# Optimization experiments

Hardware: AMD Instinct MI355X
Metric: run time of the kernel (lower is better)

Reference implementation:

```python
import jax, jax.numpy as jnp
import numpy as np

MAX_ITER = 20
F_TOL = 1e-6
FREE_NUM = 64  # free_idx[1] + 1
TRUNC = (0, 512)  # truncate_idx


def setup_inputs() -> dict:
    key = jax.random.key(0)
    ks = jax.random.split(key, 8)
    bsz, in_dim, hid, out_dim, m = 1024, 512, 1024, 256, 128
    return {
        "b_primal": jax.random.normal(ks[0], (bsz, in_dim), jnp.float32),
        "W0": jax.random.normal(ks[1], (hid, in_dim), jnp.float32) / np.sqrt(in_dim).astype(np.float32),
        "b0": jnp.zeros((hid,), jnp.float32),
        "W1": jax.random.normal(ks[2], (hid, hid), jnp.float32) / np.sqrt(hid).astype(np.float32),
        "b1": jnp.zeros((hid,), jnp.float32),
        "W2": jax.random.normal(ks[3], (out_dim, hid), jnp.float32) / np.sqrt(hid).astype(np.float32),
        "b2": jnp.zeros((out_dim,), jnp.float32),
        "A": jax.random.normal(ks[4], (m, out_dim), jnp.float32) * 0.1,
        "b_vec": jax.random.normal(ks[5], (m,), jnp.float32),
        # scaled so spectral norm < 1 -> contracting fixed-point iteration
        "WzProj": jax.random.normal(ks[6], (out_dim, out_dim), jnp.float32) * 0.03,
        "WbProj": jax.random.normal(ks[7], (out_dim, m), jnp.float32) * 0.1,
    }


def reference(b_primal, W0, b0, W1, b1, W2, b2, A, b_vec, WzProj, WbProj):
    # eval-mode forward of DualNN (report_projection=True)
    x = b_primal[:, TRUNC[0]:TRUNC[1]]
    h = jax.nn.relu(x @ W0.T + b0)
    h = jax.nn.relu(h @ W1.T + b1)
    out = h @ W2.T + b2                      # [bsz, output_dim]

    bias_proj = b_vec @ WbProj.T             # [output_dim]

    def cond(state):
        _, it, res = state
        return (it <= MAX_ITER) & (res > F_TOL)

    def body(state):
        z, it, _ = state
        z = bias_proj + z @ WzProj.T         # affine projection step
        u = z[:, :FREE_NUM]
        v = jax.nn.relu(z[:, FREE_NUM:])     # clamp non-free coordinates
        z = jnp.concatenate([u, v], axis=-1)
        res = jnp.max(jnp.abs(z @ A.T - b_vec))  # inf-norm equality residual
        return z, it + 1, res

    z_star, curr_iter, _ = jax.lax.while_loop(
        cond, body, (out, jnp.int32(1), jnp.float32(jnp.inf)))
    return (z_star, out, curr_iter)
```

## Files before the change

### kernel.cpp

```cpp
#include <hip/hip_runtime.h>

typedef __attribute__((ext_vector_type(8))) __bf16 bf16x8;
typedef __attribute__((ext_vector_type(4))) float f32x4;

#define MAX_ITER_N 20
#define F_TOL_F 1e-6f
#define FREE_NUM_N 64

#define BSZ 1024
#define IN_DIM 512
#define HID 1024
#define OUT_DIM 256
#define M_CON 128

#define WS_BAR   0
#define WS_RES   8
#define WS_BP    48
#define WS_H1    304
#define WS_H2    (WS_H1 + 524288)
#define WS_APC   (WS_H2 + 524288)
#define WS_W0C   (WS_APC + 262144)
#define WS_W1C   (WS_W0C + 262144)
#define WS_W2C   (WS_W1C + 524288)
#define WS_WZG   (WS_W2C + 131072)
#define WS_AG    (WS_WZG + 32768)

__device__ __forceinline__ unsigned short f2bf(float f) {
    unsigned int u = __float_as_uint(f);
    u += 0x7fffu + ((u >> 16) & 1u);
    return (unsigned short)(u >> 16);
}

__device__ __forceinline__ void gload_lds16(const unsigned short* g, unsigned short* l) {
    __builtin_amdgcn_global_load_lds(
        (const __attribute__((address_space(1))) unsigned int*)(const void*)g,
        (__attribute__((address_space(3))) unsigned int*)(void*)l, 16, 0, 0);
}

__global__ __launch_bounds__(256) void prep_k(
    const float* __restrict__ b_primal, const float* __restrict__ W0,
    const float* __restrict__ W1, const float* __restrict__ W2,
    const float* __restrict__ Wz, const float* __restrict__ Am,
    const float* __restrict__ b_vec, const float* __restrict__ WbProj,
    float* __restrict__ ws)
{
    unsigned short* APc = (unsigned short*)(ws + WS_APC);
    unsigned short* W0c = (unsigned short*)(ws + WS_W0C);
    unsigned short* W1c = (unsigned short*)(ws + WS_W1C);
    unsigned short* W2c = (unsigned short*)(ws + WS_W2C);
    unsigned short* WzG = (unsigned short*)(ws + WS_WZG);
    unsigned short* AG  = (unsigned short*)(ws + WS_AG);
    float* bp = ws + WS_BP;

    int b = blockIdx.x;
    int tid = threadIdx.x;
    if (b >= 2400) {
        if (tid < 48) ((unsigned int*)ws)[tid] = 0u;
        float s = 0.0f;
        for (int k = 0; k < M_CON; ++k) s += b_vec[k] * WbProj[tid * M_CON + k];
        bp[tid] = s;
        return;
    }
    const float* src; unsigned short* dst; int off;
    if (b < 512)       { src = b_primal; dst = APc; off = b; }
    else if (b < 1024) { src = W0; dst = W0c; off = b - 512; }
    else if (b < 2048) { src = W1; dst = W1c; off = b - 1024; }
    else if (b < 2304) { src = W2; dst = W2c; off = b - 2048; }
    else if (b < 2368) { src = Wz; dst = WzG; off = b - 2304; }
    else               { src = Am; dst = AG;  off = b - 2368; }
    int idx = off * 1024 + tid * 4;
    float4 v = *(const float4*)(src + idx);
    ushort4 o;
    o.x = f2bf(v.x); o.y = f2bf(v.y); o.z = f2bf(v.z); o.w = f2bf(v.w);
    *(ushort4*)(dst + idx) = o;
}

__device__ __forceinline__ bf16x8 frag128(const unsigned short* lds, int row, int gc) {
    int phys = gc ^ (row & 15);
    return __builtin_bit_cast(bf16x8, *(const uint4*)(lds + row * 128 + phys * 8));
}

template<int K, int NTN, bool RELU, bool F32OUT>
__global__ __launch_bounds__(256, 2) void gemm64_k(
    const unsigned short* __restrict__ A,
    const unsigned short* __restrict__ B,
    const float* __restrict__ bias,
    void* __restrict__ Cv, int N_)
{
    constexpr int NCH = K / 128;
    __shared__ __align__(16) unsigned short As[2][64 * 128];
    __shared__ __align__(16) unsigned short Bs[2][64 * 128];

    const int tid = threadIdx.x;
    const int w = tid >> 6;
    const int lane = tid & 63;
    const int ln = lane & 15;
    const int q  = lane >> 4;
    const int wr = w >> 1;
    const int wc = w & 1;
    const int row0 = (blockIdx.x / NTN) * 64;
    const int col0 = (blockIdx.x % NTN) * 64;
    const unsigned short* Ab = A + row0 * K;
    const unsigned short* Bb = B + col0 * K;

    int soff[4], dbase[4];
#pragma unroll
    for (int i = 0; i < 4; ++i) {
        int P = w * 256 + i * 64 + lane;
        int row = P >> 4, pgc = P & 15;
        soff[i]  = row * K + (pgc ^ (row & 15)) * 8;
        dbase[i] = (w * 256 + i * 64) * 8;
    }

    f32x4 acc[2][2];
#pragma unroll
    for (int rm = 0; rm < 2; ++rm)
#pragma unroll
        for (int cn = 0; cn < 2; ++cn)
            acc[rm][cn] = (f32x4){0.f, 0.f, 0.f, 0.f};

#pragma unroll
    for (int i = 0; i < 4; ++i) {
        gload_lds16(Ab + soff[i], &As[0][dbase[i]]);
        gload_lds16(Bb + soff[i], &Bs[0][dbase[i]]);
    }

    for (int c = 0; c < NCH; ++c) {
        __syncthreads();
        if (c + 1 < NCH) {
            const unsigned short* Ak = Ab + (c + 1) * 128;
            const unsigned short* Bk = Bb + (c + 1) * 128;
            int nb = (c + 1) & 1;
#pragma unroll
            for (int i = 0; i < 4; ++i) {
                gload_lds16(Ak + soff[i], &As[nb][dbase[i]]);
                gload_lds16(Bk + soff[i], &Bs[nb][dbase[i]]);
            }
        }
        const unsigned short* Ac = As[c & 1];
        const unsigned short* Bc = Bs[c & 1];
#pragma unroll
        for (int ks = 0; ks < 4; ++ks) {
            bf16x8 af0 = frag128(Ac, wr * 32 + ln,      ks * 4 + q);
            bf16x8 af1 = frag128(Ac, wr * 32 + 16 + ln, ks * 4 + q);
            bf16x8 bf0 = frag128(Bc, wc * 32 + ln,      ks * 4 + q);
            bf16x8 bf1 = frag128(Bc, wc * 32 + 16 + ln, ks * 4 + q);
            acc[0][0] = __builtin_amdgcn_mfma_f32_16x16x32_bf16(af0, bf0, acc[0][0], 0, 0, 0);
            acc[0][1] = __builtin_amdgcn_mfma_f32_16x16x32_bf16(af0, bf1, acc[0][1], 0, 0, 0);
            acc[1][0] = __builtin_amdgcn_mfma_f32_16x16x32_bf16(af1, bf0, acc[1][0], 0, 0, 0);
            acc[1][1] = __builtin_amdgcn_mfma_f32_16x16x32_bf16(af1, bf1, acc[1][1], 0, 0, 0);
        }
    }

#pragma unroll
    for (int cn = 0; cn < 2; ++cn) {
        const int cc = col0 + wc * 32 + cn * 16 + ln;
        const float bv = bias[cc];
#pragma unroll
        for (int rm = 0; rm < 2; ++rm)
#pragma unroll
            for (int i = 0; i < 4; ++i) {
                int r = row0 + wr * 32 + rm * 16 + q * 4 + i;
                float v = acc[rm][cn][i] + bv;
                if (RELU) v = fmaxf(v, 0.0f);
                if (F32OUT) ((float*)Cv)[r * N_ + cc] = v;
                else ((unsigned short*)Cv)[r * N_ + cc] = f2bf(v);
            }
    }
}

template<int K, int NTN, bool RELU, bool F32OUT>
__global__ __launch_bounds__(256, 4) void gemm32_k(
    const unsigned short* __restrict__ A,
    const unsigned short* __restrict__ B,
    const float* __restrict__ bias,
    void* __restrict__ Cv, int N_)
{
    constexpr int NCH = K / 128;
    __shared__ __align__(16) unsigned short As[2][32 * 128];
    __shared__ __align__(16) unsigned short Bs[2][32 * 128];

    const int tid = threadIdx.x;
    const int w = tid >> 6;
    const int lane = tid & 63;
    const int ln = lane & 15;
    const int q  = lane >> 4;
    const int wr = w >> 1;
    const int wc = w & 1;
    const int row0 = (blockIdx.x / NTN) * 32;
    const int col0 = (blockIdx.x % NTN) * 32;
    const unsigned short* Ab = A + row0 * K;
    const unsigned short* Bb = B + col0 * K;

    int soff[2], dbase[2];
#pragma unroll
    for (int i = 0; i < 2; ++i) {
        int P = w * 128 + i * 64 + lane;
        int row = P >> 4, pgc = P & 15;
        soff[i]  = row * K + (pgc ^ (row & 15)) * 8;
        dbase[i] = (w * 128 + i * 64) * 8;
    }

    f32x4 acc = {0.f, 0.f, 0.f, 0.f};

#pragma unroll
    for (int i = 0; i < 2; ++i) {
        gload_lds16(Ab + soff[i], &As[0][dbase[i]]);
        gload_lds16(Bb + soff[i], &Bs[0][dbase[i]]);
    }

    for (int c = 0; c < NCH; ++c) {
        __syncthreads();
        if (c + 1 < NCH) {
            const unsigned short* Ak = Ab + (c + 1) * 128;
            const unsigned short* Bk = Bb + (c + 1) * 128;
            int nb = (c + 1) & 1;
#pragma unroll
            for (int i = 0; i < 2; ++i) {
                gload_lds16(Ak + soff[i], &As[nb][dbase[i]]);
                gload_lds16(Bk + soff[i], &Bs[nb][dbase[i]]);
            }
        }
        const unsigned short* Ac = As[c & 1];
        const unsigned short* Bc = Bs[c & 1];
#pragma unroll
        for (int ks = 0; ks < 4; ++ks) {
            bf16x8 af = frag128(Ac, wr * 16 + ln, ks * 4 + q);
            bf16x8 bf = frag128(Bc, wc * 16 + ln, ks * 4 + q);
            acc = __builtin_amdgcn_mfma_f32_16x16x32_bf16(af, bf, acc, 0, 0, 0);
        }
    }

    const int c = col0 + wc * 16 + ln;
    const float bv = bias[c];
#pragma unroll
    for (int i = 0; i < 4; ++i) {
        int r = row0 + wr * 16 + q * 4 + i;
        float v = acc[i] + bv;
        if (RELU) v = fmaxf(v, 0.0f);
        if (F32OUT) ((float*)Cv)[r * N_ + c] = v;
        else ((unsigned short*)Cv)[r * N_ + c] = f2bf(v);
    }
}

__global__ __launch_bounds__(256, 1) void loop_k(
    const float* __restrict__ b_vec, const float* __restrict__ WzProj,
    float* __restrict__ out, float* __restrict__ ws)
{
    __shared__ __align__(16) unsigned char smem[16 * 257 * 4 + 64];
    unsigned int* done = (unsigned int*)ws;
    unsigned int* res = (unsigned int*)(ws + WS_RES);
    float* bp = ws + WS_BP;
    const unsigned short* WzG = (const unsigned short*)(ws + WS_WZG);
    const unsigned short* AG  = (const unsigned short*)(ws + WS_AG);
    float* outz = out + BSZ * OUT_DIM;

    const int tid  = threadIdx.x;
    const int wave = tid >> 6;
    const int lane = tid & 63;
    const int ln   = lane & 15;
    const int q    = lane >> 4;
    const int r0   = blockIdx.x * 16;

    unsigned short (*zS)[264] = (unsigned short(*)[264])smem;
    float* red = (float*)(smem + 16 * 257 * 4);

    {
        int row = tid >> 4;
        int c0  = (tid & 15) * 16;
        const float* src = outz + (r0 + row) * OUT_DIM + c0;
#pragma unroll
        for (int i = 0; i < 4; ++i) {
            float4 v = *(const float4*)(src + i * 4);
            ushort4 o;
            o.x = f2bf(v.x); o.y = f2bf(v.y); o.z = f2bf(v.z); o.w = f2bf(v.w);
            *(ushort4*)&zS[row][c0 + i * 4] = o;
        }
    }

    bf16x8 afr[2][8];
    float bvv[2];
#pragma unroll
    for (int mt = 0; mt < 2; ++mt) {
        int m = wave * 32 + mt * 16 + ln;
        bvv[mt] = b_vec[m];
#pragma unroll
        for (int ks = 0; ks < 8; ++ks)
            afr[mt][ks] = __builtin_bit_cast(bf16x8, *(const uint4*)(AG + m * OUT_DIM + ks * 32 + q * 8));
    }
    int colg[4];
    float bpv[4];
    bf16x8 wzfr[4][8];
#pragma unroll
    for (int nt = 0; nt < 4; ++nt) {
        colg[nt] = wave * 64 + nt * 16 + ln;
        bpv[nt]  = bp[colg[nt]];
#pragma unroll
        for (int ks = 0; ks < 8; ++ks)
            wzfr[nt][ks] = __builtin_bit_cast(bf16x8, *(const uint4*)(WzG + colg[nt] * OUT_DIM + ks * 32 + q * 8));
    }
    __syncthreads();

    bf16x8 zfr[8];
#pragma unroll
    for (int ks = 0; ks < 8; ++ks)
        zfr[ks] = __builtin_bit_cast(bf16x8, *(const uint4*)&zS[ln][ks * 32 + q * 8]);

    const f32x4 zero4 = {0.f, 0.f, 0.f, 0.f};

    for (int t = 1; t <= MAX_ITER_N; ++t) {
        f32x4 acc[4];
        f32x4 acc2[2];
#pragma unroll
        for (int nt = 0; nt < 4; ++nt) acc[nt] = zero4;
        acc2[0] = zero4; acc2[1] = zero4;
#pragma unroll
        for (int ks = 0; ks < 8; ++ks) {
#pragma unroll
            for (int nt = 0; nt < 4; ++nt)
                acc[nt] = __builtin_amdgcn_mfma_f32_16x16x32_bf16(zfr[ks], wzfr[nt][ks], acc[nt], 0, 0, 0);
            if (t > 1) {
#pragma unroll
                for (int mt = 0; mt < 2; ++mt)
                    acc2[mt] = __builtin_amdgcn_mfma_f32_16x16x32_bf16(zfr[ks], afr[mt][ks], acc2[mt], 0, 0, 0);
            }
        }
        float vals[4][4];
#pragma unroll
        for (int nt = 0; nt < 4; ++nt)
#pragma unroll
            for (int i = 0; i < 4; ++i) {
                float v = acc[nt][i] + bpv[nt];
                if (colg[nt] >= FREE_NUM_N) v = fmaxf(v, 0.0f);
                vals[nt][i] = v;
            }
        if (t > 1) {
            float lmax = 0.0f;
#pragma unroll
            for (int mt = 0; mt < 2; ++mt)
#pragma unroll
                for (int i = 0; i < 4; ++i)
                    lmax = fmaxf(lmax, fabsf(acc2[mt][i] - bvv[mt]));
#pragma unroll
            for (int off = 32; off > 0; off >>= 1)
                lmax = fmaxf(lmax, __shfl_xor(lmax, off));
            if (lane == 0) red[wave] = lmax;
        }
        if (t == MAX_ITER_N) {
#pragma unroll
            for (int nt = 0; nt < 4; ++nt)
#pragma unroll
                for (int i = 0; i < 4; ++i)
                    out[(r0 + q * 4 + i) * OUT_DIM + colg[nt]] = vals[nt][i];
        }
        __syncthreads();
        if (t > 1 && tid == 0) {
            float bm = fmaxf(fmaxf(red[0], red[1]), fmaxf(red[2], red[3]));
            atomicMax(res + (t - 2), __float_as_uint(bm));
        }
#pragma unroll
        for (int nt = 0; nt < 4; ++nt)
#pragma unroll
            for (int i = 0; i < 4; ++i)
                zS[q * 4 + i][colg[nt]] = f2bf(vals[nt][i]);
        __syncthreads();
#pragma unroll
        for (int ks = 0; ks < 8; ++ks)
            zfr[ks] = __builtin_bit_cast(bf16x8, *(const uint4*)&zS[ln][ks * 32 + q * 8]);
    }

    {
        f32x4 acc2[2];
        acc2[0] = zero4; acc2[1] = zero4;
#pragma unroll
        for (int ks = 0; ks < 8; ++ks)
#pragma unroll
            for (int mt = 0; mt < 2; ++mt)
                acc2[mt] = __builtin_amdgcn_mfma_f32_16x16x32_bf16(zfr[ks], afr[mt][ks], acc2[mt], 0, 0, 0);
        float lmax = 0.0f;
#pragma unroll
        for (int mt = 0; mt < 2; ++mt)
#pragma unroll
            for (int i = 0; i < 4; ++i)
                lmax = fmaxf(lmax, fabsf(acc2[mt][i] - bvv[mt]));
#pragma unroll
        for (int off = 32; off > 0; off >>= 1)
            lmax = fmaxf(lmax, __shfl_xor(lmax, off));
        if (lane == 0) red[wave] = lmax;
        __syncthreads();
        if (tid == 0) {
            float bm = fmaxf(fmaxf(red[0], red[1]), fmaxf(red[2], red[3]));
            atomicMax(res + (MAX_ITER_N - 1), __float_as_uint(bm));
            __threadfence();
            atomicAdd(done, 1u);
            while (__hip_atomic_load(done, __ATOMIC_ACQUIRE, __HIP_MEMORY_SCOPE_AGENT) < 64u)
                __builtin_amdgcn_s_sleep(2);
        }
        __syncthreads();
    }

    int T;
    {
        float rv = 1e30f;
        if (tid < MAX_ITER_N)
            rv = __uint_as_float(__hip_atomic_load(res + tid, __ATOMIC_ACQUIRE, __HIP_MEMORY_SCOPE_AGENT));
        if (tid < 64) {
            unsigned long long m = __ballot((tid < MAX_ITER_N) && !(rv > F_TOL_F));
            if (tid == 0) red[0] = (float)(m ? (int)__ffsll(m) : MAX_ITER_N);
        }
        __syncthreads();
        T = (int)red[0];
    }
    if (blockIdx.x == 0 && tid == 0)
        out[2 * BSZ * OUT_DIM] = (float)(T + 1);
    if (T >= MAX_ITER_N) return;

    float (*zF)[257] = (float(*)[257])smem;
    {
        const int row = tid >> 4;
        const int c0 = (tid & 15) * 16;
        for (int i = 0; i < 16; ++i)
            zF[row][c0 + i] = outz[(r0 + row) * OUT_DIM + c0 + i];
        __syncthreads();
        const int j = tid;
        const float bj = bp[j];
        for (int t = 0; t < T; ++t) {
            float acc[16] = {};
            for (int k = 0; k < OUT_DIM; ++k) {
                float wv = WzProj[j * OUT_DIM + k];
#pragma unroll
                for (int r = 0; r < 16; ++r) acc[r] += zF[r][k] * wv;
            }
            __syncthreads();
#pragma unroll
            for (int r = 0; r < 16; ++r) {
                float v = acc[r] + bj;
                if (j >= FREE_NUM_N) v = fmaxf(v, 0.0f);
                zF[r][j] = v;
            }
            __syncthreads();
        }
        for (int i = 0; i < 16; ++i)
            out[(r0 + row) * OUT_DIM + c0 + i] = zF[row][c0 + i];
    }
}

extern "C" void kernel_launch(void* const* d_in, const int* in_sizes, int n_in,
                              void* d_out, int out_size, void* d_ws, size_t ws_size,
                              hipStream_t stream) {
    const float* b_primal = (const float*)d_in[0];
    const float* W0     = (const float*)d_in[1];
    const float* b0     = (const float*)d_in[2];
    const float* W1     = (const float*)d_in[3];
    const float* b1     = (const float*)d_in[4];
    const float* W2     = (const float*)d_in[5];
    const float* b2     = (const float*)d_in[6];
    const float* Amat   = (const float*)d_in[7];
    const float* b_vec  = (const float*)d_in[8];
    const float* WzProj = (const float*)d_in[9];
    const float* WbProj = (const float*)d_in[10];
    float* out = (float*)d_out;
    float* ws  = (float*)d_ws;

    unsigned short* h1c = (unsigned short*)(ws + WS_H1);
    unsigned short* h2c = (unsigned short*)(ws + WS_H2);
    unsigned short* APc = (unsigned short*)(ws + WS_APC);
    unsigned short* W0c = (unsigned short*)(ws + WS_W0C);
    unsigned short* W1c = (unsigned short*)(ws + WS_W1C);
    unsigned short* W2c = (unsigned short*)(ws + WS_W2C);
    float* outz = out + BSZ * OUT_DIM;

    hipLaunchKernelGGL(prep_k, dim3(2401), dim3(256), 0, stream,
                       b_primal, W0, W1, W2, WzProj, Amat, b_vec, WbProj, ws);

    hipLaunchKernelGGL((gemm64_k<IN_DIM, 16, true, false>), dim3(256), dim3(256), 0, stream,
                       APc, W0c, b0, (void*)h1c, HID);
    hipLaunchKernelGGL((gemm64_k<HID, 16, true, false>), dim3(256), dim3(256), 0, stream,
                       h1c, W1c, b1, (void*)h2c, HID);
    hipLaunchKernelGGL((gemm32_k<HID, 8, false, true>), dim3(256), dim3(256), 0, stream,
                       h2c, W2c, b2, (void*)outz, OUT_DIM);

    hipLaunchKernelGGL(loop_k, dim3(64), dim3(256), 0, stream, b_vec, WzProj, out, ws);
}
```

Baseline: 142.4 us.

## Fuse prep, MLP GEMMs and fixed-point loop into one persistent kernel

Replaces five separate kernel launches (bf16 conversion, three GEMMs, iteration loop) with one persistent 256-block kernel that separates the stages with software grid barriers built on an atomic counter. Counters are zeroed by a memset before launch. The aim is to remove launch gaps and tail effects between the small stages. In exchange, all stages run at one block per CU with a single 64KB shared buffer, and the design depends on all 256 blocks being co-resident so the spin barriers cannot deadlock.

```diff
diff --git a/kernel.cpp b/kernel.cpp
--- a/kernel.cpp
+++ b/kernel.cpp
@@ -13,7 +13,8 @@
 #define OUT_DIM 256
 #define M_CON 128
 
-#define WS_BAR   0
+#define WS_DONE  0
+#define WS_GCNT  1
 #define WS_RES   8
 #define WS_BP    48
 #define WS_H1    304
@@ -37,60 +38,30 @@
         (__attribute__((address_space(3))) unsigned int*)(void*)l, 16, 0, 0);
 }
 
-__global__ __launch_bounds__(256) void prep_k(
-    const float* __restrict__ b_primal, const float* __restrict__ W0,
-    const float* __restrict__ W1, const float* __restrict__ W2,
-    const float* __restrict__ Wz, const float* __restrict__ Am,
-    const float* __restrict__ b_vec, const float* __restrict__ WbProj,
-    float* __restrict__ ws)
-{
-    unsigned short* APc = (unsigned short*)(ws + WS_APC);
-    unsigned short* W0c = (unsigned short*)(ws + WS_W0C);
-    unsigned short* W1c = (unsigned short*)(ws + WS_W1C);
-    unsigned short* W2c = (unsigned short*)(ws + WS_W2C);
-    unsigned short* WzG = (unsigned short*)(ws + WS_WZG);
-    unsigned short* AG  = (unsigned short*)(ws + WS_AG);
-    float* bp = ws + WS_BP;
-
-    int b = blockIdx.x;
-    int tid = threadIdx.x;
-    if (b >= 2400) {
-        if (tid < 48) ((unsigned int*)ws)[tid] = 0u;
-        float s = 0.0f;
-        for (int k = 0; k < M_CON; ++k) s += b_vec[k] * WbProj[tid * M_CON + k];
-        bp[tid] = s;
-        return;
-    }
-    const float* src; unsigned short* dst; int off;
-    if (b < 512)       { src = b_primal; dst = APc; off = b; }
-    else if (b < 1024) { src = W0; dst = W0c; off = b - 512; }
-    else if (b < 2048) { src = W1; dst = W1c; off = b - 1024; }
-    else if (b < 2304) { src = W2; dst = W2c; off = b - 2048; }
-    else if (b < 2368) { src = Wz; dst = WzG; off = b - 2304; }
-    else               { src = Am; dst = AG;  off = b - 2368; }
-    int idx = off * 1024 + tid * 4;
-    float4 v = *(const float4*)(src + idx);
-    ushort4 o;
-    o.x = f2bf(v.x); o.y = f2bf(v.y); o.z = f2bf(v.z); o.w = f2bf(v.w);
-    *(ushort4*)(dst + idx) = o;
-}
-
 __device__ __forceinline__ bf16x8 frag128(const unsigned short* lds, int row, int gc) {
     int phys = gc ^ (row & 15);
     return __builtin_bit_cast(bf16x8, *(const uint4*)(lds + row * 128 + phys * 8));
 }
 
-template<int K, int NTN, bool RELU, bool F32OUT>
-__global__ __launch_bounds__(256, 2) void gemm64_k(
-    const unsigned short* __restrict__ A,
-    const unsigned short* __restrict__ B,
-    const float* __restrict__ bias,
-    void* __restrict__ Cv, int N_)
+__device__ __forceinline__ void gbar(unsigned int* gcnt, unsigned int target) {
+    __syncthreads();
+    __threadfence();
+    if (threadIdx.x == 0) {
+        atomicAdd(gcnt, 1u);
+        while (__hip_atomic_load(gcnt, __ATOMIC_RELAXED, __HIP_MEMORY_SCOPE_AGENT) < target)
+            __builtin_amdgcn_s_sleep(1);
+    }
+    __syncthreads();
+    __threadfence();
+}
+
+template<int K, bool RELU, bool F32OUT>
+__device__ __forceinline__ void gemm64_dev(
+    const unsigned short* __restrict__ A, const unsigned short* __restrict__ B,
+    const float* __restrict__ bias, void* __restrict__ Cv, int N_,
+    int row0, int col0, unsigned short* sA, unsigned short* sB)
 {
     constexpr int NCH = K / 128;
-    __shared__ __align__(16) unsigned short As[2][64 * 128];
-    __shared__ __align__(16) unsigned short Bs[2][64 * 128];
-
     const int tid = threadIdx.x;
     const int w = tid >> 6;
     const int lane = tid & 63;
@@ -98,8 +69,6 @@
     const int q  = lane >> 4;
     const int wr = w >> 1;
     const int wc = w & 1;
-    const int row0 = (blockIdx.x / NTN) * 64;
-    const int col0 = (blockIdx.x % NTN) * 64;
     const unsigned short* Ab = A + row0 * K;
     const unsigned short* Bb = B + col0 * K;
 
@@ -121,8 +90,8 @@
 
 #pragma unroll
     for (int i = 0; i < 4; ++i) {
-        gload_lds16(Ab + soff[i], &As[0][dbase[i]]);
-        gload_lds16(Bb + soff[i], &Bs[0][dbase[i]]);
+        gload_lds16(Ab + soff[i], sA + dbase[i]);
+        gload_lds16(Bb + soff[i], sB + dbase[i]);
     }
 
     for (int c = 0; c < NCH; ++c) {
@@ -130,15 +99,15 @@
         if (c + 1 < NCH) {
             const unsigned short* Ak = Ab + (c + 1) * 128;
             const unsigned short* Bk = Bb + (c + 1) * 128;
-            int nb = (c + 1) & 1;
+            int nb = ((c + 1) & 1) * 8192;
 #pragma unroll
             for (int i = 0; i < 4; ++i) {
-                gload_lds16(Ak + soff[i], &As[nb][dbase[i]]);
-                gload_lds16(Bk + soff[i], &Bs[nb][dbase[i]]);
-            }
-        }
-        const unsigned short* Ac = As[c & 1];
-        const unsigned short* Bc = Bs[c & 1];
+                gload_lds16(Ak + soff[i], sA + nb + dbase[i]);
+                gload_lds16(Bk + soff[i], sB + nb + dbase[i]);
+            }
+        }
+        const unsigned short* Ac = sA + (c & 1) * 8192;
+        const unsigned short* Bc = sB + (c & 1) * 8192;
 #pragma unroll
         for (int ks = 0; ks < 4; ++ks) {
             bf16x8 af0 = frag128(Ac, wr * 32 + ln,      ks * 4 + q);
@@ -169,17 +138,13 @@
     }
 }
 
-template<int K, int NTN, bool RELU, bool F32OUT>
-__global__ __launch_bounds__(256, 4) void gemm32_k(
-    const unsigned short* __restrict__ A,
-    const unsigned short* __restrict__ B,
-    const float* __restrict__ bias,
-    void* __restrict__ Cv, int N_)
+template<int K, bool RELU, bool F32OUT>
+__device__ __forceinline__ void gemm32_dev(
+    const unsigned short* __restrict__ A, const unsigned short* __restrict__ B,
+    const float* __restrict__ bias, void* __restrict__ Cv, int N_,
+    int row0, int col0, unsigned short* sA, unsigned short* sB)
 {
     constexpr int NCH = K / 128;
-    __shared__ __align__(16) unsigned short As[2][32 * 128];
-    __shared__ __align__(16) unsigned short Bs[2][32 * 128];
-
     const int tid = threadIdx.x;
     const int w = tid >> 6;
     const int lane = tid & 63;
@@ -187,8 +152,6 @@
     const int q  = lane >> 4;
     const int wr = w >> 1;
     const int wc = w & 1;
-    const int row0 = (blockIdx.x / NTN) * 32;
-    const int col0 = (blockIdx.x % NTN) * 32;
     const unsigned short* Ab = A + row0 * K;
     const unsigned short* Bb = B + col0 * K;
 
@@ -205,8 +168,8 @@
 
 #pragma unroll
     for (int i = 0; i < 2; ++i) {
-        gload_lds16(Ab + soff[i], &As[0][dbase[i]]);
-        gload_lds16(Bb + soff[i], &Bs[0][dbase[i]]);
+        gload_lds16(Ab + soff[i], sA + dbase[i]);
+        gload_lds16(Bb + soff[i], sB + dbase[i]);
     }
 
     for (int c = 0; c < NCH; ++c) {
@@ -214,15 +177,15 @@
         if (c + 1 < NCH) {
             const unsigned short* Ak = Ab + (c + 1) * 128;
             const unsigned short* Bk = Bb + (c + 1) * 128;
-            int nb = (c + 1) & 1;
+            int nb = ((c + 1) & 1) * 4096;
 #pragma unroll
             for (int i = 0; i < 2; ++i) {
-                gload_lds16(Ak + soff[i], &As[nb][dbase[i]]);
-                gload_lds16(Bk + soff[i], &Bs[nb][dbase[i]]);
-            }
-        }
-        const unsigned short* Ac = As[c & 1];
-        const unsigned short* Bc = Bs[c & 1];
+                gload_lds16(Ak + soff[i], sA + nb + dbase[i]);
+                gload_lds16(Bk + soff[i], sB + nb + dbase[i]);
+            }
+        }
+        const unsigned short* Ac = sA + (c & 1) * 4096;
+        const unsigned short* Bc = sB + (c & 1) * 4096;
 #pragma unroll
         for (int ks = 0; ks < 4; ++ks) {
             bf16x8 af = frag128(Ac, wr * 16 + ln, ks * 4 + q);
@@ -231,39 +194,92 @@
         }
     }
 
-    const int c = col0 + wc * 16 + ln;
-    const float bv = bias[c];
+    const int cc = col0 + wc * 16 + ln;
+    const float bv = bias[cc];
 #pragma unroll
     for (int i = 0; i < 4; ++i) {
         int r = row0 + wr * 16 + q * 4 + i;
         float v = acc[i] + bv;
         if (RELU) v = fmaxf(v, 0.0f);
-        if (F32OUT) ((float*)Cv)[r * N_ + c] = v;
-        else ((unsigned short*)Cv)[r * N_ + c] = f2bf(v);
-    }
-}
-
-__global__ __launch_bounds__(256, 1) void loop_k(
+        if (F32OUT) ((float*)Cv)[r * N_ + cc] = v;
+        else ((unsigned short*)Cv)[r * N_ + cc] = f2bf(v);
+    }
+}
+
+__global__ __launch_bounds__(256, 1) void fused_k(
+    const float* __restrict__ b_primal, const float* __restrict__ W0,
+    const float* __restrict__ b0v, const float* __restrict__ W1,
+    const float* __restrict__ b1v, const float* __restrict__ W2,
+    const float* __restrict__ b2v, const float* __restrict__ Am,
     const float* __restrict__ b_vec, const float* __restrict__ WzProj,
+    const float* __restrict__ WbProj,
     float* __restrict__ out, float* __restrict__ ws)
 {
-    __shared__ __align__(16) unsigned char smem[16 * 257 * 4 + 64];
-    unsigned int* done = (unsigned int*)ws;
-    unsigned int* res = (unsigned int*)(ws + WS_RES);
+    __shared__ __align__(16) unsigned char smem[65536];
+
+    unsigned int* done = (unsigned int*)ws + WS_DONE;
+    unsigned int* gcnt = (unsigned int*)ws + WS_GCNT;
+    unsigned int* res  = (unsigned int*)(ws + WS_RES);
     float* bp = ws + WS_BP;
-    const unsigned short* WzG = (const unsigned short*)(ws + WS_WZG);
-    const unsigned short* AG  = (const unsigned short*)(ws + WS_AG);
+    unsigned short* h1c = (unsigned short*)(ws + WS_H1);
+    unsigned short* h2c = (unsigned short*)(ws + WS_H2);
+    unsigned short* APc = (unsigned short*)(ws + WS_APC);
+    unsigned short* W0c = (unsigned short*)(ws + WS_W0C);
+    unsigned short* W1c = (unsigned short*)(ws + WS_W1C);
+    unsigned short* W2c = (unsigned short*)(ws + WS_W2C);
+    unsigned short* WzG = (unsigned short*)(ws + WS_WZG);
+    unsigned short* AG  = (unsigned short*)(ws + WS_AG);
     float* outz = out + BSZ * OUT_DIM;
 
-    const int tid  = threadIdx.x;
+    const int tid = threadIdx.x;
+    const int bid = blockIdx.x;
+
+    unsigned short* sA = (unsigned short*)smem;
+    unsigned short* sB = (unsigned short*)(smem + 32768);
+
+    for (int u = bid; u < 2400; u += 256) {
+        const float* src; unsigned short* dst; int off;
+        if (u < 512)       { src = b_primal; dst = APc; off = u; }
+        else if (u < 1024) { src = W0;     dst = W0c; off = u - 512; }
+        else if (u < 2048) { src = W1;     dst = W1c; off = u - 1024; }
+        else if (u < 2304) { src = W2;     dst = W2c; off = u - 2048; }
+        else if (u < 2368) { src = WzProj; dst = WzG; off = u - 2304; }
+        else               { src = Am;     dst = AG;  off = u - 2368; }
+        int idx = off * 1024 + tid * 4;
+        float4 v = *(const float4*)(src + idx);
+        ushort4 o;
+        o.x = f2bf(v.x); o.y = f2bf(v.y); o.z = f2bf(v.z); o.w = f2bf(v.w);
+        *(ushort4*)(dst + idx) = o;
+    }
+    if (bid == 0) {
+        float s = 0.0f;
+        for (int k = 0; k < M_CON; ++k) s += b_vec[k] * WbProj[tid * M_CON + k];
+        bp[tid] = s;
+    }
+    gbar(gcnt, 256);
+
+    gemm64_dev<IN_DIM, true, false>(APc, W0c, b0v, (void*)h1c, HID,
+                                    (bid >> 4) * 64, (bid & 15) * 64, sA, sB);
+    gbar(gcnt, 512);
+
+    gemm64_dev<HID, true, false>(h1c, W1c, b1v, (void*)h2c, HID,
+                                 (bid >> 4) * 64, (bid & 15) * 64, sA, sB);
+    gbar(gcnt, 768);
+
+    gemm32_dev<HID, false, true>(h2c, W2c, b2v, (void*)outz, OUT_DIM,
+                                 (bid >> 3) * 32, (bid & 7) * 32, sA, sB);
+    gbar(gcnt, 1024);
+
+    if (bid >= 64) return;
+
     const int wave = tid >> 6;
     const int lane = tid & 63;
     const int ln   = lane & 15;
     const int q    = lane >> 4;
-    const int r0   = blockIdx.x * 16;
+    const int r0   = bid * 16;
 
     unsigned short (*zS)[264] = (unsigned short(*)[264])smem;
-    float* red = (float*)(smem + 16 * 257 * 4);
+    float* red = (float*)(smem + 60928);
 
     {
         int row = tid >> 4;
@@ -411,7 +427,7 @@
         __syncthreads();
         T = (int)red[0];
     }
-    if (blockIdx.x == 0 && tid == 0)
+    if (bid == 0 && tid == 0)
         out[2 * BSZ * OUT_DIM] = (float)(T + 1);
     if (T >= MAX_ITER_N) return;
 
@@ -462,23 +478,9 @@
     float* out = (float*)d_out;
     float* ws  = (float*)d_ws;
 
-    unsigned short* h1c = (unsigned short*)(ws + WS_H1);
-    unsigned short* h2c = (unsigned short*)(ws + WS_H2);
-    unsigned short* APc = (unsigned short*)(ws + WS_APC);
-    unsigned short* W0c = (unsigned short*)(ws + WS_W0C);
-    unsigned short* W1c = (unsigned short*)(ws + WS_W1C);
-    unsigned short* W2c = (unsigned short*)(ws + WS_W2C);
-    float* outz = out + BSZ * OUT_DIM;
-
-    hipLaunchKernelGGL(prep_k, dim3(2401), dim3(256), 0, stream,
-                       b_primal, W0, W1, W2, WzProj, Amat, b_vec, WbProj, ws);
-
-    hipLaunchKernelGGL((gemm64_k<IN_DIM, 16, true, false>), dim3(256), dim3(256), 0, stream,
-                       APc, W0c, b0, (void*)h1c, HID);
-    hipLaunchKernelGGL((gemm64_k<HID, 16, true, false>), dim3(256), dim3(256), 0, stream,
-                       h1c, W1c, b1, (void*)h2c, HID);
-    hipLaunchKernelGGL((gemm32_k<HID, 8, false, true>), dim3(256), dim3(256), 0, stream,
-                       h2c, W2c, b2, (void*)outz, OUT_DIM);
-
-    hipLaunchKernelGGL(loop_k, dim3(64), dim3(256), 0, stream, b_vec, WzProj, out, ws);
-}
+    hipMemsetAsync(ws, 0, 192, stream);
+
+    hipLaunchKernelGGL(fused_k, dim3(256), dim3(256), 0, stream,
+                       b_primal, W0, b0, W1, b1, W2, b2, Amat, b_vec,
+                       WzProj, WbProj, out, ws);
+}
```

New measurement: 324.4 us. 2.28x slower.
